# Optimization experiments

Hardware: AMD Instinct MI355X
Metric: run time of the kernel (lower is better)

Reference implementation:

```python
import jax, jax.numpy as jnp
import numpy as np

B, T, H = 2, 2048, 1024
NH_R, HD_R = 4, 256            # RWKV6 heads / head_dim
EXP, HD_M = 2, 64
DI = EXP * H                   # mamba inner = 2048
NH_M = DI // HD_M              # 32 mamba heads
DS = 128                       # mamba d_state
CK = 4                         # causal conv kernel
FFN = 4 * H
EPS = 1e-6


def rms(x, w, eps=EPS):
    return w * x * jax.lax.rsqrt(jnp.mean(x * x, -1, keepdims=True) + eps)


def setup_inputs() -> dict:
    key = jax.random.key(0)
    ks = iter(jax.random.split(key, 32))
    def w(shape, scale=0.02):
        return jax.random.normal(next(ks), shape, jnp.float32) * scale
    return dict(
        x=w((B, T, H), 1.0),
        ln_w=jnp.ones((H,), jnp.float32),
        r_w=w((H, H)), k_w=w((H, H)), v_w=w((H, H)), g_w=w((H, H)), dw_w=w((H, H)),
        u=w((NH_R, HD_R), 0.5),
        gn_w=jnp.ones((H,), jnp.float32),
        o_w=w((H, H)),
        in_proj=w((H, 2 * DI + 2 * DS + NH_M)),
        conv_w=w((DI + 2 * DS, CK), 0.1),
        conv_b=jnp.zeros((DI + 2 * DS,), jnp.float32),
        dt_bias=w((NH_M,), 0.1),
        A_log=jnp.log(jnp.arange(1, NH_M + 1, dtype=jnp.float32)),
        D_m=w((NH_M,), 0.5),
        m_norm_w=jnp.ones((DI,), jnp.float32),
        out_proj=w((DI, H)),
        gate_w=jnp.zeros((2 * H, 1), jnp.float32),   # zero-init per module
        gate_b=jnp.zeros((1,), jnp.float32),         # logit(0.5) = 0
        ffn_ln_w=jnp.ones((H,), jnp.float32),
        ffn_w1=w((H, FFN)),
        ffn_w2=w((FFN, H)),
    )


def _rwkv6(nx, r_w, k_w, v_w, g_w, dw_w, u, gn_w, o_w):
    r = (nx @ r_w).reshape(B, T, NH_R, HD_R)
    k = (nx @ k_w).reshape(B, T, NH_R, HD_R)
    v = (nx @ v_w).reshape(B, T, NH_R, HD_R)
    g = jax.nn.silu(nx @ g_w)                                  # output gate
    wdec = jnp.exp(-jnp.exp(nx @ dw_w)).reshape(B, T, NH_R, HD_R)  # data-dep decay in (0,1)
    tm = lambda a: a.transpose(1, 0, 2, 3)                     # [T,B,h,d]

    def step(S, inp):  # S: [B,h,K,V]
        rt, kt, vt, wt = inp
        kv = kt[..., :, None] * vt[..., None, :]
        o = jnp.einsum('bhk,bhkv->bhv', rt, S + u[..., :, None] * kv)
        return wt[..., :, None] * S + kv, o

    S0 = jnp.zeros((B, NH_R, HD_R, HD_R), nx.dtype)
    _, o = jax.lax.scan(step, S0, (tm(r), tm(k), tm(v), tm(wdec)))
    o = o.transpose(1, 0, 2, 3)                                # [B,T,h,d]
    o = o * jax.lax.rsqrt(jnp.mean(o * o, -1, keepdims=True) + EPS)  # per-head RMS (group norm)
    o = o.reshape(B, T, H) * gn_w
    return (o * g) @ o_w


def _mamba2(nx, in_proj, conv_w, conv_b, dt_bias, A_log, D_m, m_norm_w, out_proj):
    zxbcdt = nx @ in_proj
    z, xBC, dt = jnp.split(zxbcdt, [DI, 2 * DI + 2 * DS], axis=-1)
    xp = jnp.pad(xBC, ((0, 0), (CK - 1, 0), (0, 0)))           # causal depthwise conv
    xBC = sum(xp[:, i:i + T, :] * conv_w[:, i] for i in range(CK)) + conv_b
    xBC = jax.nn.silu(xBC)
    xm, Bm, Cm = jnp.split(xBC, [DI, DI + DS], axis=-1)
    xm = xm.reshape(B, T, NH_M, HD_M)
    dt = jax.nn.softplus(dt + dt_bias)                          # [B,T,nh]
    A = -jnp.exp(A_log)                                         # [nh]

    def step(h, inp):  # h: [B,nh,hd,ds]
        xt, Bt, Ct, dtt = inp
        h = h * jnp.exp(dtt * A)[..., None, None] + (dtt[..., None] * xt)[..., None] * Bt[:, None, None, :]
        y = jnp.einsum('bhds,bs->bhd', h, Ct)
        return h, y

    h0 = jnp.zeros((B, NH_M, HD_M, DS), nx.dtype)
    _, y = jax.lax.scan(step, h0, (xm.transpose(1, 0, 2, 3), Bm.transpose(1, 0, 2), Cm.transpose(1, 0, 2), dt.transpose(1, 0, 2)))
    y = y.transpose(1, 0, 2, 3) + D_m[None, None, :, None] * xm
    y = y.reshape(B, T, DI)
    y = rms(y * jax.nn.silu(z), m_norm_w)                       # gated RMSNorm
    return y @ out_proj


def reference(x, ln_w, r_w, k_w, v_w, g_w, dw_w, u, gn_w, o_w,
              in_proj, conv_w, conv_b, dt_bias, A_log, D_m, m_norm_w, out_proj,
              gate_w, gate_b, ffn_ln_w, ffn_w1, ffn_w2):
    nx = rms(x, ln_w)
    o_r = _rwkv6(nx, r_w, k_w, v_w, g_w, dw_w, u, gn_w, o_w)
    o_m = _mamba2(nx, in_proj, conv_w, conv_b, dt_bias, A_log, D_m, m_norm_w, out_proj)
    gate = jax.nn.sigmoid(jnp.concatenate([o_r, o_m], -1) @ gate_w + gate_b)  # [B,T,1]
    x = x + gate * o_r + (1.0 - gate) * o_m
    x = x + jax.nn.gelu(rms(x, ffn_ln_w) @ ffn_w1, approximate=False) @ ffn_w2
    return x
```

## Files before the change

kernel.cpp:

```cpp
#include <hip/hip_runtime.h>
#include <hip/hip_bf16.h>
#include <stdint.h>

#define B_ 2
#define T_ 2048
#define H_ 1024
#define M_ 4096
#define DI 2048
#define DS 128
#define CONVD 2304
#define LD2 4480
#define EPS_ 1e-6f

typedef __bf16 bf16x8 __attribute__((ext_vector_type(8)));
typedef float f32x4 __attribute__((ext_vector_type(4)));
typedef uint32_t u32x4 __attribute__((ext_vector_type(4)));

__device__ __forceinline__ unsigned short f2bfu(float f) {
    union { float f; uint32_t u; } a; a.f = f;
    uint32_t r = a.u + 0x7FFFu + ((a.u >> 16) & 1u);
    return (unsigned short)(r >> 16);
}
__device__ __forceinline__ float bfu2f(unsigned short u) {
    union { uint32_t u; float f; } a; a.u = ((uint32_t)u) << 16; return a.f;
}
__device__ __forceinline__ float siluf(float x) { return x / (1.f + expf(-x)); }
__device__ __forceinline__ bf16x8 zero8() { bf16x8 r{}; return r; }

__global__ __launch_bounds__(256) void k_rms1024(const float* __restrict__ in, const float* __restrict__ w,
                                                 unsigned short* __restrict__ out) {
    __shared__ float red[4];
    int m = blockIdx.x, tid = threadIdx.x;
    size_t base = (size_t)m * H_ + tid * 4;
    float4 v = *(const float4*)(in + base);
    float ss = v.x * v.x + v.y * v.y + v.z * v.z + v.w * v.w;
#pragma unroll
    for (int off = 32; off; off >>= 1) ss += __shfl_xor(ss, off);
    if ((tid & 63) == 0) red[tid >> 6] = ss;
    __syncthreads();
    float scale = rsqrtf((red[0] + red[1] + red[2] + red[3]) * (1.f / 1024.f) + EPS_);
    float4 wv = *(const float4*)(w + tid * 4);
    ushort4 o;
    o.x = f2bfu(v.x * wv.x * scale); o.y = f2bfu(v.y * wv.y * scale);
    o.z = f2bfu(v.z * wv.z * scale); o.w = f2bfu(v.w * wv.w * scale);
    *(ushort4*)(out + base) = o;
}

__global__ __launch_bounds__(256) void k_transpose(const float* __restrict__ src, unsigned short* __restrict__ dst,
                                                   int K, int N, int NP) {
    __shared__ float t[32][33];
    int n0 = blockIdx.x * 32, k0 = blockIdx.y * 32;
    int tx = threadIdx.x & 31, ty = threadIdx.x >> 5;
#pragma unroll
    for (int i = ty; i < 32; i += 8) {
        int k = k0 + i, n = n0 + tx;
        t[i][tx] = (n < N) ? src[(size_t)k * N + n] : 0.f;
    }
    __syncthreads();
#pragma unroll
    for (int i = ty; i < 32; i += 8) {
        int n = n0 + i, k = k0 + tx;
        if (n < NP) dst[(size_t)n * K + k] = f2bfu(t[tx][i]);
    }
}

template <int EPI>
__global__ __launch_bounds__(256) void k_gemm(const unsigned short* __restrict__ A, const unsigned short* __restrict__ Bt,
                                              void* __restrict__ Cout, const float* __restrict__ aux,
                                              int M, int N, int K) {
    __shared__ alignas(16) unsigned short As[128 * 64];
    __shared__ alignas(16) unsigned short Bs[128 * 64];
    const int tid = threadIdx.x;
    const int m0 = blockIdx.y * 128, n0 = blockIdx.x * 128;
    const int wave = tid >> 6, lane = tid & 63;
    const int wm = (wave >> 1) * 64, wn = (wave & 1) * 64;
    const int fr = lane & 15, fg = lane >> 4;
    const int srow = tid >> 3;
    const int ske = (tid & 7) * 8;

    f32x4 acc[4][4];
#pragma unroll
    for (int m = 0; m < 4; m++)
#pragma unroll
        for (int n = 0; n < 4; n++) acc[m][n] = (f32x4)(0.f);

    const int nk = K >> 6;
    u32x4 ra[4], rb[4];
#pragma unroll
    for (int i = 0; i < 4; i++) {
        ra[i] = *(const u32x4*)(A + (size_t)(m0 + srow + 32 * i) * K + ske);
        rb[i] = *(const u32x4*)(Bt + (size_t)(n0 + srow + 32 * i) * K + ske);
    }
    for (int kt = 0; kt < nk; ++kt) {
        __syncthreads();
#pragma unroll
        for (int i = 0; i < 4; i++) {
            int lin = (tid + 256 * i) * 16;
            int sw = lin ^ (((lin >> 7) & 7) << 4);
            *(u32x4*)((char*)As + sw) = ra[i];
            *(u32x4*)((char*)Bs + sw) = rb[i];
        }
        __syncthreads();
        if (kt + 1 < nk) {
#pragma unroll
            for (int i = 0; i < 4; i++) {
                ra[i] = *(const u32x4*)(A + (size_t)(m0 + srow + 32 * i) * K + (kt + 1) * 64 + ske);
                rb[i] = *(const u32x4*)(Bt + (size_t)(n0 + srow + 32 * i) * K + (kt + 1) * 64 + ske);
            }
        }
#pragma unroll
        for (int ks = 0; ks < 2; ++ks) {
            bf16x8 af[4], bg[4];
#pragma unroll
            for (int m = 0; m < 4; m++) {
                int row = wm + m * 16 + fr;
                int lin = row * 128 + ks * 64 + fg * 16;
                af[m] = *(const bf16x8*)((const char*)As + (lin ^ ((row & 7) << 4)));
            }
#pragma unroll
            for (int n = 0; n < 4; n++) {
                int col = wn + n * 16 + fr;
                int lin = col * 128 + ks * 64 + fg * 16;
                bg[n] = *(const bf16x8*)((const char*)Bs + (lin ^ ((col & 7) << 4)));
            }
#pragma unroll
            for (int m = 0; m < 4; m++)
#pragma unroll
                for (int n = 0; n < 4; n++)
                    acc[m][n] = __builtin_amdgcn_mfma_f32_16x16x32_bf16(af[m], bg[n], acc[m][n], 0, 0, 0);
        }
    }
#pragma unroll
    for (int m = 0; m < 4; m++) {
#pragma unroll
        for (int r = 0; r < 4; r++) {
            size_t row = (size_t)(m0 + wm + m * 16 + fg * 4 + r);
#pragma unroll
            for (int n = 0; n < 4; n++) {
                size_t idx = row * N + n0 + wn + n * 16 + fr;
                float v = acc[m][n][r];
                if constexpr (EPI == 0) ((float*)Cout)[idx] = v;
                else if constexpr (EPI == 4) ((unsigned short*)Cout)[idx] = f2bfu(0.5f * v * (1.f + erff(v * 0.70710678118f)));
                else ((float*)Cout)[idx] = v + aux[idx];
            }
        }
    }
}

__global__ __launch_bounds__(256) void k_gemm_fused(const unsigned short* __restrict__ A, const unsigned short* __restrict__ Bt,
                                                    unsigned short* __restrict__ RB, unsigned short* __restrict__ KB,
                                                    unsigned short* __restrict__ VB, unsigned short* __restrict__ GB,
                                                    float* __restrict__ WF, unsigned short* __restrict__ C2B) {
    __shared__ alignas(16) unsigned short As[128 * 64];
    __shared__ alignas(16) unsigned short Bs[128 * 64];
    const int tid = threadIdx.x;
    const int m0 = blockIdx.y * 128, n0 = blockIdx.x * 128;
    const int wave = tid >> 6, lane = tid & 63;
    const int wm = (wave >> 1) * 64, wn = (wave & 1) * 64;
    const int fr = lane & 15, fg = lane >> 4;
    const int srow = tid >> 3;
    const int ske = (tid & 7) * 8;
    const int K = 1024;

    f32x4 acc[4][4];
#pragma unroll
    for (int m = 0; m < 4; m++)
#pragma unroll
        for (int n = 0; n < 4; n++) acc[m][n] = (f32x4)(0.f);

    u32x4 ra[4], rb[4];
#pragma unroll
    for (int i = 0; i < 4; i++) {
        ra[i] = *(const u32x4*)(A + (size_t)(m0 + srow + 32 * i) * K + ske);
        rb[i] = *(const u32x4*)(Bt + (size_t)(n0 + srow + 32 * i) * K + ske);
    }
    for (int kt = 0; kt < 16; ++kt) {
        __syncthreads();
#pragma unroll
        for (int i = 0; i < 4; i++) {
            int lin = (tid + 256 * i) * 16;
            int sw = lin ^ (((lin >> 7) & 7) << 4);
            *(u32x4*)((char*)As + sw) = ra[i];
            *(u32x4*)((char*)Bs + sw) = rb[i];
        }
        __syncthreads();
        if (kt + 1 < 16) {
#pragma unroll
            for (int i = 0; i < 4; i++) {
                ra[i] = *(const u32x4*)(A + (size_t)(m0 + srow + 32 * i) * K + (kt + 1) * 64 + ske);
                rb[i] = *(const u32x4*)(Bt + (size_t)(n0 + srow + 32 * i) * K + (kt + 1) * 64 + ske);
            }
        }
#pragma unroll
        for (int ks = 0; ks < 2; ++ks) {
            bf16x8 af[4], bg[4];
#pragma unroll
            for (int m = 0; m < 4; m++) {
                int row = wm + m * 16 + fr;
                int lin = row * 128 + ks * 64 + fg * 16;
                af[m] = *(const bf16x8*)((const char*)As + (lin ^ ((row & 7) << 4)));
            }
#pragma unroll
            for (int n = 0; n < 4; n++) {
                int col = wn + n * 16 + fr;
                int lin = col * 128 + ks * 64 + fg * 16;
                bg[n] = *(const bf16x8*)((const char*)Bs + (lin ^ ((col & 7) << 4)));
            }
#pragma unroll
            for (int m = 0; m < 4; m++)
#pragma unroll
                for (int n = 0; n < 4; n++)
                    acc[m][n] = __builtin_amdgcn_mfma_f32_16x16x32_bf16(af[m], bg[n], acc[m][n], 0, 0, 0);
        }
    }
    const int seg = n0 >> 10;
#pragma unroll
    for (int m = 0; m < 4; m++) {
#pragma unroll
        for (int r = 0; r < 4; r++) {
            size_t row = (size_t)(m0 + wm + m * 16 + fg * 4 + r);
#pragma unroll
            for (int n = 0; n < 4; n++) {
                int gcol = n0 + wn + n * 16 + fr;
                float v = acc[m][n][r];
                if (n0 < 5120) {
                    size_t idx = row * 1024 + (gcol & 1023);
                    if (seg == 0) RB[idx] = f2bfu(v);
                    else if (seg == 1) KB[idx] = f2bfu(v);
                    else if (seg == 2) VB[idx] = f2bfu(v);
                    else if (seg == 3) GB[idx] = f2bfu(siluf(v));
                    else WF[idx] = expf(-expf(v));
                } else {
                    C2B[row * 4480 + (gcol - 5120)] = f2bfu(v);
                }
            }
        }
    }
}

__global__ __launch_bounds__(256) void k_rwkv_prep(unsigned short* __restrict__ RB, unsigned short* __restrict__ KB,
                                                   const float* __restrict__ WF, const float* __restrict__ u,
                                                   unsigned short* __restrict__ KDt, unsigned short* __restrict__ QLb,
                                                   float* __restrict__ DDb) {
    __shared__ float red[16][257];
    __shared__ float red2[16][17];
    const int c = blockIdx.x, bh = blockIdx.y;
    const int b = bh >> 2, h = bh & 3;
    const int k = threadIdx.x;
    const size_t m0 = (size_t)b * T_ + c * 16;
    const int hk = h * 256 + k;
    const float uv = u[hk];
    float Q = 1.f;
    float kd[16];
#pragma unroll
    for (int s = 0; s < 16; s++) {
        size_t off = (m0 + s) * H_ + hk;
        float r = bfu2f(RB[off]);
        float kv = bfu2f(KB[off]);
        float w = WF[off];
        RB[off] = f2bfu(r * Q);
        Q = fmaxf(Q * w, 1e-35f);
        float kdv = kv / Q;
        kd[s] = kdv;
        KB[off] = f2bfu(kdv);
        red[s][k] = r * uv * kv;
    }
    QLb[((size_t)(b * 128 + c)) * 1024 + hk] = f2bfu(Q);
    size_t kt0 = (((size_t)(b * 128 + c)) * 1024 + hk) * 16;
#pragma unroll
    for (int s = 0; s < 16; s++) KDt[kt0 + s] = f2bfu(kd[s]);
    __syncthreads();
    {
        int s = threadIdx.x >> 4, part = threadIdx.x & 15;
        float ps = 0.f;
#pragma unroll
        for (int j = 0; j < 16; j++) ps += red[s][part * 16 + j];
        red2[s][part] = ps;
    }
    __syncthreads();
    if (threadIdx.x < 32) {
        int s = threadIdx.x & 15, half = threadIdx.x >> 4;
        float d = 0.f;
#pragma unroll
        for (int j = 0; j < 8; j++) d += red2[s][half * 8 + j];
        DDb[(((size_t)bh * 128 + c) * 2 + half) * 16 + s] = d;
    }
}

__global__ __launch_bounds__(256) void k_rwkv_carry(const unsigned short* __restrict__ KD, const unsigned short* __restrict__ VB,
                                                    const unsigned short* __restrict__ QLb, unsigned short* __restrict__ Scc) {
    __shared__ unsigned short kds[16][256];
    __shared__ float lv[16][4];
    const int vg = blockIdx.x, bh = blockIdx.y;
    const int b = bh >> 2, h = bh & 3;
    const int k = threadIdx.x;
    const int hk = h * 256 + k;
    const size_t baseM = (size_t)b * T_;
    float s0 = 0.f, s1 = 0.f, s2 = 0.f, s3 = 0.f;
    for (int c = 0; c < 128; ++c) {
        size_t m0 = baseM + c * 16;
        if ((c & 7) == 0 && c > 0) {
            int cc = c >> 3;
            size_t sb = ((size_t)(bh * 16 + cc) * 256 + vg * 4) * 256 + k;
            Scc[sb] = f2bfu(s0); Scc[sb + 256] = f2bfu(s1);
            Scc[sb + 512] = f2bfu(s2); Scc[sb + 768] = f2bfu(s3);
        }
        __syncthreads();
#pragma unroll
        for (int it = 0; it < 2; ++it) {
            int i = threadIdx.x + it * 256;
            int row = i >> 5, col8 = (i & 31) * 8;
            *(u32x4*)&kds[row][col8] = *(const u32x4*)(KD + (m0 + row) * H_ + h * 256 + col8);
        }
        if (threadIdx.x < 64) {
            int t = threadIdx.x >> 2, j = threadIdx.x & 3;
            lv[t][j] = bfu2f(VB[(m0 + t) * H_ + h * 256 + vg * 4 + j]);
        }
        __syncthreads();
        float a0 = 0.f, a1 = 0.f, a2 = 0.f, a3 = 0.f;
#pragma unroll
        for (int t = 0; t < 16; t++) {
            float kdv = bfu2f(kds[t][k]);
            a0 = fmaf(kdv, lv[t][0], a0);
            a1 = fmaf(kdv, lv[t][1], a1);
            a2 = fmaf(kdv, lv[t][2], a2);
            a3 = fmaf(kdv, lv[t][3], a3);
        }
        float ql = bfu2f(QLb[((size_t)(b * 128 + c)) * 1024 + hk]);
        s0 = (s0 + a0) * ql; s1 = (s1 + a1) * ql;
        s2 = (s2 + a2) * ql; s3 = (s3 + a3) * ql;
    }
}

__global__ __launch_bounds__(256) void k_rwkv_out(const unsigned short* __restrict__ RT, const unsigned short* __restrict__ KD,
                                                  const unsigned short* __restrict__ KDt, const unsigned short* __restrict__ VB,
                                                  const unsigned short* __restrict__ QLb, const float* __restrict__ DDb,
                                                  const unsigned short* __restrict__ Scc,
                                                  float* __restrict__ P0, float* __restrict__ P1) {
    __shared__ unsigned short Sb[64][136];
    __shared__ unsigned short VT[64][24];
    __shared__ unsigned short Ab[16][24];
    __shared__ float dls[16];
    const int tid = threadIdx.x;
    const int vt = blockIdx.x, cc = blockIdx.y;
    const int bh = blockIdx.z >> 1, kh = blockIdx.z & 1;
    const int b = bh >> 2, h = bh & 3;
    const int wave = tid >> 6, lane = tid & 63;
    const int l16 = lane & 15, lq = lane >> 4;
    const int wv0 = wave * 16;
    const int hk0 = h * 256 + kh * 128;
    const int hv = h * 256 + vt * 64;
    const int aoff = (lq < 2) ? lq * 8 : 0;
    float* __restrict__ OP = kh ? P1 : P0;
    f32x4 sreg[8];
    if (cc == 0) {
#pragma unroll
        for (int kt = 0; kt < 8; kt++) sreg[kt] = (f32x4)(0.f);
        for (int i = tid; i < 64 * 136 / 8; i += 256) ((u32x4*)Sb)[i] = (u32x4)(0u);
    } else {
        size_t sbase = ((size_t)(bh * 16 + cc) * 256 + vt * 64);
        for (int i = tid; i < 1024; i += 256) {
            int v = i >> 4, k8 = (i & 15) * 8;
            *(u32x4*)&Sb[v][k8] = *(const u32x4*)(Scc + (sbase + v) * 256 + kh * 128 + k8);
        }
#pragma unroll
        for (int kt = 0; kt < 8; kt++) {
            ushort4 w4 = *(const ushort4*)(Scc + (sbase + wv0 + l16) * 256 + kh * 128 + kt * 16 + lq * 4);
            sreg[kt][0] = bfu2f(w4.x); sreg[kt][1] = bfu2f(w4.y);
            sreg[kt][2] = bfu2f(w4.z); sreg[kt][3] = bfu2f(w4.w);
        }
    }
    __syncthreads();

    for (int fc = 0; fc < 8; ++fc) {
        const int c = cc * 8 + fc;
        const size_t m0 = (size_t)b * T_ + c * 16;
        const size_t bc = (size_t)(b * 128 + c);
        if (fc > 0) __syncthreads();
        {
            int st = tid >> 4, v4 = (tid & 15) * 4;
            ushort4 v4v = *(const ushort4*)(VB + (m0 + st) * H_ + hv + v4);
            VT[v4 + 0][st] = v4v.x; VT[v4 + 1][st] = v4v.y;
            VT[v4 + 2][st] = v4v.z; VT[v4 + 3][st] = v4v.w;
            if (tid < 16) dls[tid] = DDb[(((size_t)bh * 128 + c) * 2 + kh) * 16 + tid];
        }
        __syncthreads();
        const size_t rowA = (m0 + l16) * H_ + hk0;
        bf16x8 rtf[4];
#pragma unroll
        for (int ks = 0; ks < 4; ks++) rtf[ks] = *(const bf16x8*)(RT + rowA + ks * 32 + lq * 8);
        f32x4 Aacc = (f32x4)(0.f);
#pragma unroll
        for (int ks = 0; ks < 4; ks++) {
            bf16x8 kdf = *(const bf16x8*)(KD + rowA + ks * 32 + lq * 8);
            Aacc = __builtin_amdgcn_mfma_f32_16x16x32_bf16(rtf[ks], kdf, Aacc, 0, 0, 0);
        }
        f32x4 oacc = (f32x4)(0.f);
#pragma unroll
        for (int ks = 0; ks < 4; ks++) {
            bf16x8 sbf = *(const bf16x8*)(&Sb[wv0 + l16][ks * 32 + lq * 8]);
            oacc = __builtin_amdgcn_mfma_f32_16x16x32_bf16(rtf[ks], sbf, oacc, 0, 0, 0);
        }
#pragma unroll
        for (int r = 0; r < 4; r++) {
            int t = lq * 4 + r, s = l16;
            float av = (s < t) ? Aacc[r] : ((s == t) ? dls[t] : 0.f);
            Ab[t][s] = f2bfu(av);
        }
        bf16x8 abf_t = *(const bf16x8*)(&Ab[l16][aoff]);
        bf16x8 vtf_t = *(const bf16x8*)(&VT[wv0 + l16][aoff]);
        bf16x8 abf = (lq < 2) ? abf_t : zero8();
        bf16x8 vtf = (lq < 2) ? vtf_t : zero8();
        oacc = __builtin_amdgcn_mfma_f32_16x16x32_bf16(abf, vtf, oacc, 0, 0, 0);
#pragma unroll
        for (int r = 0; r < 4; r++)
            OP[(m0 + lq * 4 + r) * H_ + hv + wv0 + l16] = oacc[r];
#pragma unroll
        for (int kt = 0; kt < 8; kt++) {
            const unsigned short* kp = KDt + (((bc * 1024) + hk0 + kt * 16 + l16) << 4) + aoff;
            bf16x8 kdtf_t = *(const bf16x8*)kp;
            bf16x8 kdtf = (lq < 2) ? kdtf_t : zero8();
            sreg[kt] = __builtin_amdgcn_mfma_f32_16x16x32_bf16(kdtf, vtf, sreg[kt], 0, 0, 0);
            ushort4 q4 = *(const ushort4*)(QLb + bc * 1024 + hk0 + kt * 16 + lq * 4);
            sreg[kt][0] *= bfu2f(q4.x); sreg[kt][1] *= bfu2f(q4.y);
            sreg[kt][2] *= bfu2f(q4.z); sreg[kt][3] *= bfu2f(q4.w);
            ushort4 pk;
            pk.x = f2bfu(sreg[kt][0]); pk.y = f2bfu(sreg[kt][1]);
            pk.z = f2bfu(sreg[kt][2]); pk.w = f2bfu(sreg[kt][3]);
            *(ushort4*)(&Sb[wv0 + l16][kt * 16 + lq * 4]) = pk;
        }
    }
}

__global__ __launch_bounds__(256) void k_rwkv_post(const float* __restrict__ P0, const float* __restrict__ P1,
                                                   const float* __restrict__ gn_w, unsigned short* __restrict__ g_io) {
    int m = blockIdx.x, tid = threadIdx.x;
    int wave = tid >> 6, lane = tid & 63;
    size_t base = (size_t)m * H_ + wave * 256 + lane * 4;
    int col = wave * 256 + lane * 4;
    float4 a = *(const float4*)(P0 + base);
    float4 b4 = *(const float4*)(P1 + base);
    float4 v; v.x = a.x + b4.x; v.y = a.y + b4.y; v.z = a.z + b4.z; v.w = a.w + b4.w;
    float ss = v.x * v.x + v.y * v.y + v.z * v.z + v.w * v.w;
#pragma unroll
    for (int off = 32; off; off >>= 1) ss += __shfl_xor(ss, off);
    float scale = rsqrtf(ss * (1.f / 256.f) + EPS_);
    float4 gn = *(const float4*)(gn_w + col);
    ushort4 gb4 = *(const ushort4*)(g_io + base);
    ushort4 out;
    out.x = f2bfu(v.x * scale * gn.x * bfu2f(gb4.x));
    out.y = f2bfu(v.y * scale * gn.y * bfu2f(gb4.y));
    out.z = f2bfu(v.z * scale * gn.z * bfu2f(gb4.z));
    out.w = f2bfu(v.w * scale * gn.w * bfu2f(gb4.w));
    *(ushort4*)(g_io + base) = out;
}

__global__ __launch_bounds__(256) void k_conv(const unsigned short* __restrict__ C2B, const float* __restrict__ conv_w,
                                              const float* __restrict__ conv_b, unsigned short* __restrict__ XB,
                                              float* __restrict__ BCF) {
    int m = blockIdx.y;
    int c = blockIdx.x * 256 + threadIdx.x;
    int b = m >> 11, t = m & 2047;
    float acc = conv_b[c];
#pragma unroll
    for (int i = 0; i < 4; i++) {
        int tt = t - 3 + i;
        if (tt >= 0) acc = fmaf(bfu2f(C2B[((size_t)(b * T_ + tt)) * LD2 + DI + c]), conv_w[c * 4 + i], acc);
    }
    float r = siluf(acc);
    if (c < DI) XB[(size_t)m * DI + c] = f2bfu(r);
    else BCF[(size_t)m * 256 + (c - DI)] = r;
}

#define MT 32
__global__ __launch_bounds__(256, 2) void k_mamba_scan(const unsigned short* __restrict__ C2B, const unsigned short* __restrict__ XB,
                                                       const float* __restrict__ BCF,
                                                       const float* __restrict__ dt_bias, const float* __restrict__ A_log,
                                                       unsigned short* __restrict__ Y0, unsigned short* __restrict__ Y1) {
    __shared__ float lB[MT][68], lC[MT][68], lx[MT][16], lda[MT], ldt[MT];
    __shared__ float pst[MT * 272];
    const int tid = threadIdx.x;
    const int d0 = blockIdx.x * 16;
    const int sh = blockIdx.y;
    const int bh = blockIdx.z;
    const int b = bh >> 5, h = bh & 31;
    const int wave = tid >> 6, lane = tid & 63;
    const int dloc = wave * 4 + (lane >> 4);
    const int li = lane & 15;
    const size_t baseM = (size_t)b * T_;
    const float A = -expf(A_log[h]);
    const float dtb = dt_bias[h];
    unsigned short* __restrict__ YP = sh ? Y1 : Y0;
    float hS[4] = {0.f, 0.f, 0.f, 0.f};

    for (int c = 0; c < T_ / MT; ++c) {
        __syncthreads();
        int t0 = c * MT;
#pragma unroll
        for (int it = 0; it < 2; ++it) {
            int idx = (tid + it * 256) * 4;
            int tt = idx >> 6, s = idx & 63;
            const float* src = BCF + (baseM + t0 + tt) * 256 + sh * 64 + s;
            *(float4*)&lB[tt][s] = *(const float4*)(src);
            *(float4*)&lC[tt][s] = *(const float4*)(src + 128);
        }
#pragma unroll
        for (int it = 0; it < 2; ++it) {
            int idx = tid + it * 256;
            int tt = idx >> 4, i = idx & 15;
            lx[tt][i] = bfu2f(XB[(baseM + t0 + tt) * DI + h * 64 + d0 + i]);
        }
        if (tid < MT) {
            float draw = bfu2f(C2B[(baseM + t0 + tid) * LD2 + 4352 + h]) + dtb;
            float ds = draw > 20.f ? draw : log1pf(expf(draw));
            ldt[tid] = ds;
            lda[tid] = expf(A * ds);
        }
        __syncthreads();
#pragma unroll 1
        for (int tt = 0; tt < MT; ++tt) {
            float da = lda[tt];
            float dtx = ldt[tt] * lx[tt][dloc];
            float4 Bv = *(const float4*)&lB[tt][li * 4];
            float4 Cv = *(const float4*)&lC[tt][li * 4];
            hS[0] = fmaf(hS[0], da, dtx * Bv.x);
            hS[1] = fmaf(hS[1], da, dtx * Bv.y);
            hS[2] = fmaf(hS[2], da, dtx * Bv.z);
            hS[3] = fmaf(hS[3], da, dtx * Bv.w);
            float p0 = fmaf(hS[1], Cv.y, hS[0] * Cv.x);
            float p1 = fmaf(hS[3], Cv.w, hS[2] * Cv.z);
            pst[tt * 272 + dloc * 17 + li] = p0 + p1;
        }
        __syncthreads();
        {
            int tt = tid >> 3, dl = tid & 7;
            const float* row0 = &pst[tt * 272 + dl * 17];
            const float* row1 = &pst[tt * 272 + (dl + 8) * 17];
            float s0 = 0.f, s1 = 0.f;
#pragma unroll
            for (int j = 0; j < 16; j++) { s0 += row0[j]; s1 += row1[j]; }
            size_t orow = (baseM + t0 + tt) * DI + h * 64 + d0;
            YP[orow + dl] = f2bfu(s0);
            YP[orow + dl + 8] = f2bfu(s1);
        }
    }
}

__global__ __launch_bounds__(256) void k_mamba_post(unsigned short* __restrict__ y_io, const unsigned short* __restrict__ y1,
                                                    const unsigned short* __restrict__ XB,
                                                    const unsigned short* __restrict__ C2B, const float* __restrict__ D_m,
                                                    const float* __restrict__ mnw) {
    __shared__ float red[4];
    int m = blockIdx.x, tid = threadIdx.x;
    int j0 = tid * 8;
    const float Dv = D_m[j0 >> 6];
    ushort4 ya = *(const ushort4*)(y_io + (size_t)m * DI + j0);
    ushort4 yb = *(const ushort4*)(y_io + (size_t)m * DI + j0 + 4);
    ushort4 wa = *(const ushort4*)(y1 + (size_t)m * DI + j0);
    ushort4 wb = *(const ushort4*)(y1 + (size_t)m * DI + j0 + 4);
    ushort4 xa = *(const ushort4*)(XB + (size_t)m * DI + j0);
    ushort4 xb = *(const ushort4*)(XB + (size_t)m * DI + j0 + 4);
    ushort4 za = *(const ushort4*)(C2B + (size_t)m * LD2 + j0);
    ushort4 zb = *(const ushort4*)(C2B + (size_t)m * LD2 + j0 + 4);
    float yv[8] = {bfu2f(ya.x) + bfu2f(wa.x), bfu2f(ya.y) + bfu2f(wa.y), bfu2f(ya.z) + bfu2f(wa.z), bfu2f(ya.w) + bfu2f(wa.w),
                   bfu2f(yb.x) + bfu2f(wb.x), bfu2f(yb.y) + bfu2f(wb.y), bfu2f(yb.z) + bfu2f(wb.z), bfu2f(yb.w) + bfu2f(wb.w)};
    float xv[8] = {bfu2f(xa.x), bfu2f(xa.y), bfu2f(xa.z), bfu2f(xa.w), bfu2f(xb.x), bfu2f(xb.y), bfu2f(xb.z), bfu2f(xb.w)};
    float zv[8] = {bfu2f(za.x), bfu2f(za.y), bfu2f(za.z), bfu2f(za.w), bfu2f(zb.x), bfu2f(zb.y), bfu2f(zb.z), bfu2f(zb.w)};
    float val[8];
    float ss = 0.f;
#pragma unroll
    for (int i = 0; i < 8; i++) {
        float v = (yv[i] + Dv * xv[i]) * siluf(zv[i]);
        val[i] = v;
        ss += v * v;
    }
#pragma unroll
    for (int off = 32; off; off >>= 1) ss += __shfl_xor(ss, off);
    if ((tid & 63) == 0) red[tid >> 6] = ss;
    __syncthreads();
    float scale = rsqrtf((red[0] + red[1] + red[2] + red[3]) * (1.f / 2048.f) + EPS_);
    ushort4 oa, ob;
    oa.x = f2bfu(val[0] * scale * mnw[j0 + 0]); oa.y = f2bfu(val[1] * scale * mnw[j0 + 1]);
    oa.z = f2bfu(val[2] * scale * mnw[j0 + 2]); oa.w = f2bfu(val[3] * scale * mnw[j0 + 3]);
    ob.x = f2bfu(val[4] * scale * mnw[j0 + 4]); ob.y = f2bfu(val[5] * scale * mnw[j0 + 5]);
    ob.z = f2bfu(val[6] * scale * mnw[j0 + 6]); ob.w = f2bfu(val[7] * scale * mnw[j0 + 7]);
    *(ushort4*)(y_io + (size_t)m * DI + j0) = oa;
    *(ushort4*)(y_io + (size_t)m * DI + j0 + 4) = ob;
}

__global__ __launch_bounds__(256) void k_mix(const float* __restrict__ x, const float* __restrict__ o_r,
                                             const float* __restrict__ o_m, const float* __restrict__ gw,
                                             const float* __restrict__ gb, const float* __restrict__ flnw,
                                             float* __restrict__ x1, unsigned short* __restrict__ nx2) {
    __shared__ float red[4];
    int m = blockIdx.x, tid = threadIdx.x;
    size_t base = (size_t)m * H_ + tid * 4;
    float4 orv = *(const float4*)(o_r + base);
    float4 omv = *(const float4*)(o_m + base);
    float4 xv = *(const float4*)(x + base);
    float4 g1 = *(const float4*)(gw + tid * 4);
    float4 g2 = *(const float4*)(gw + 1024 + tid * 4);
    float ps = orv.x * g1.x + orv.y * g1.y + orv.z * g1.z + orv.w * g1.w
             + omv.x * g2.x + omv.y * g2.y + omv.z * g2.z + omv.w * g2.w;
#pragma unroll
    for (int off = 32; off; off >>= 1) ps += __shfl_xor(ps, off);
    if ((tid & 63) == 0) red[tid >> 6] = ps;
    __syncthreads();
    float g = 1.f / (1.f + expf(-(red[0] + red[1] + red[2] + red[3] + gb[0])));
    float4 xo;
    xo.x = xv.x + g * orv.x + (1.f - g) * omv.x;
    xo.y = xv.y + g * orv.y + (1.f - g) * omv.y;
    xo.z = xv.z + g * orv.z + (1.f - g) * omv.z;
    xo.w = xv.w + g * orv.w + (1.f - g) * omv.w;
    *(float4*)(x1 + base) = xo;
    float ss = xo.x * xo.x + xo.y * xo.y + xo.z * xo.z + xo.w * xo.w;
#pragma unroll
    for (int off = 32; off; off >>= 1) ss += __shfl_xor(ss, off);
    __syncthreads();
    if ((tid & 63) == 0) red[tid >> 6] = ss;
    __syncthreads();
    float scale = rsqrtf((red[0] + red[1] + red[2] + red[3]) * (1.f / 1024.f) + EPS_);
    float4 wv = *(const float4*)(flnw + tid * 4);
    ushort4 o;
    o.x = f2bfu(xo.x * scale * wv.x); o.y = f2bfu(xo.y * scale * wv.y);
    o.z = f2bfu(xo.z * scale * wv.z); o.w = f2bfu(xo.w * scale * wv.w);
    *(ushort4*)(nx2 + base) = o;
}

extern "C" void kernel_launch(void* const* d_in, const int* in_sizes, int n_in,
                              void* d_out, int out_size, void* d_ws, size_t ws_size,
                              hipStream_t stream) {
    const float* x = (const float*)d_in[0];
    const float* ln_w = (const float*)d_in[1];
    const float* r_w = (const float*)d_in[2];
    const float* k_w = (const float*)d_in[3];
    const float* v_w = (const float*)d_in[4];
    const float* g_w = (const float*)d_in[5];
    const float* dw_w = (const float*)d_in[6];
    const float* u = (const float*)d_in[7];
    const float* gn_w = (const float*)d_in[8];
    const float* o_w = (const float*)d_in[9];
    const float* in_proj = (const float*)d_in[10];
    const float* conv_w = (const float*)d_in[11];
    const float* conv_b = (const float*)d_in[12];
    const float* dt_bias = (const float*)d_in[13];
    const float* A_log = (const float*)d_in[14];
    const float* D_m = (const float*)d_in[15];
    const float* m_norm_w = (const float*)d_in[16];
    const float* out_proj = (const float*)d_in[17];
    const float* gate_w = (const float*)d_in[18];
    const float* gate_b = (const float*)d_in[19];
    const float* ffn_ln_w = (const float*)d_in[20];
    const float* ffn_w1 = (const float*)d_in[21];
    const float* ffn_w2 = (const float*)d_in[22];
    (void)in_sizes; (void)n_in;

    const size_t NEEDED = 192675840ull;
    if (ws_size < NEEDED) {
        hipMemsetAsync(d_out, 0, (size_t)out_size * 4, stream);
        return;
    }
    char* ws = (char*)d_ws;
    unsigned short* WT5 = (unsigned short*)(ws + 0);
    unsigned short* INPT = (unsigned short*)(ws + 10485760);
    unsigned short* QLb = (unsigned short*)(ws + 0);
    float* DDb = (float*)(ws + 524288);
    unsigned short* SCC = (unsigned short*)(ws + 1048576);
    unsigned short* F1T = (unsigned short*)(ws + 0);
    unsigned short* F2T = (unsigned short*)(ws + 10485760);
    unsigned short* OWT = (unsigned short*)(ws + 19660800);
    unsigned short* OPT = (unsigned short*)(ws + 21757952);
    unsigned short* NXB = (unsigned short*)(ws + 25952256);
    unsigned short* KDt = NXB;
    unsigned short* RB = (unsigned short*)(ws + 34340864);
    unsigned short* KB = (unsigned short*)(ws + 42729472);
    unsigned short* VB = (unsigned short*)(ws + 51118080);
    unsigned short* GB = (unsigned short*)(ws + 59506688);
    float* WF = (float*)(ws + 67895296);
    unsigned short* Y1 = (unsigned short*)(ws + 67895296);
    float* OM = (float*)(ws + 34340864);
    unsigned short* MIDB = (unsigned short*)(ws + 51118080);
    unsigned short* C2B = (unsigned short*)(ws + 84672512);
    unsigned short* XB = (unsigned short*)(ws + 121372672);
    float* BCF = (float*)(ws + 138149888);
    float* P0 = (float*)(ws + 142344192);
    float* P1 = (float*)(ws + 159121408);
    unsigned short* YB = (unsigned short*)(ws + 175898624);

    dim3 blk(256);
    k_rms1024<<<M_, blk, 0, stream>>>(x, ln_w, NXB);
    k_transpose<<<dim3(32, 32), blk, 0, stream>>>(r_w, WT5 + 0ull * 1048576, 1024, 1024, 1024);
    k_transpose<<<dim3(32, 32), blk, 0, stream>>>(k_w, WT5 + 1ull * 1048576, 1024, 1024, 1024);
    k_transpose<<<dim3(32, 32), blk, 0, stream>>>(v_w, WT5 + 2ull * 1048576, 1024, 1024, 1024);
    k_transpose<<<dim3(32, 32), blk, 0, stream>>>(g_w, WT5 + 3ull * 1048576, 1024, 1024, 1024);
    k_transpose<<<dim3(32, 32), blk, 0, stream>>>(dw_w, WT5 + 4ull * 1048576, 1024, 1024, 1024);
    k_transpose<<<dim3(140, 32), blk, 0, stream>>>(in_proj, INPT, 1024, 4384, 4480);
    k_transpose<<<dim3(32, 32), blk, 0, stream>>>(o_w, OWT, 1024, 1024, 1024);
    k_transpose<<<dim3(32, 64), blk, 0, stream>>>(out_proj, OPT, 2048, 1024, 1024);
    k_gemm_fused<<<dim3(75, 32), blk, 0, stream>>>(NXB, WT5, RB, KB, VB, GB, WF, C2B);
    k_conv<<<dim3(9, M_), blk, 0, stream>>>(C2B, conv_w, conv_b, XB, BCF);
    k_rwkv_prep<<<dim3(128, 8), blk, 0, stream>>>(RB, KB, WF, u, KDt, QLb, DDb);
    k_rwkv_carry<<<dim3(64, 8), blk, 0, stream>>>(KB, VB, QLb, SCC);
    k_rwkv_out<<<dim3(4, 16, 16), blk, 0, stream>>>(RB, KB, KDt, VB, QLb, DDb, SCC, P0, P1);
    k_rwkv_post<<<M_, blk, 0, stream>>>(P0, P1, gn_w, GB);
    k_transpose<<<dim3(128, 32), blk, 0, stream>>>(ffn_w1, F1T, 1024, 4096, 4096);
    k_transpose<<<dim3(32, 128), blk, 0, stream>>>(ffn_w2, F2T, 4096, 1024, 1024);
    k_mamba_scan<<<dim3(4, 2, 64), blk, 0, stream>>>(C2B, XB, BCF, dt_bias, A_log, YB, Y1);
    k_mamba_post<<<M_, blk, 0, stream>>>(YB, Y1, XB, C2B, D_m, m_norm_w);
    k_gemm<0><<<dim3(8, 32), blk, 0, stream>>>(GB, OWT, P1, nullptr, 4096, 1024, 1024);
    k_gemm<0><<<dim3(8, 32), blk, 0, stream>>>(YB, OPT, OM, nullptr, 4096, 1024, 2048);
    k_mix<<<M_, blk, 0, stream>>>(x, P1, OM, gate_w, gate_b, ffn_ln_w, P0, NXB);
    k_gemm<4><<<dim3(32, 32), blk, 0, stream>>>(NXB, F1T, MIDB, nullptr, 4096, 4096, 1024);
    k_gemm<5><<<dim3(8, 32), blk, 0, stream>>>(MIDB, F2T, (float*)d_out, P0, 4096, 1024, 4096);
}
```

Measured before the change: 1.053 ms.

## Replace sequential Mamba2 scan with chunked SSD matmul formulation on MFMA

Replaces the per-timestep recurrent Mamba2 scan with a chunked state-space-duality scheme. A prep kernel computes cumulative dt and decay factors, a mask kernel builds the intra-chunk C·B^T decay matrices with MFMA, a carry kernel computes chunk-boundary states, and an output kernel combines the inter-chunk state contribution with the intra-chunk attention-like term using bf16 MFMA. The aim is to swap the long serial FMA loop for parallel matrix-core work. In exchange it adds more launches, intermediate buffers, and bf16 rounding of states and decay-weighted terms.

```diff
diff --git a/kernel.cpp b/kernel.cpp
--- a/kernel.cpp
+++ b/kernel.cpp
@@ -472,81 +472,279 @@
     else BCF[(size_t)m * 256 + (c - DI)] = r;
 }
 
-#define MT 32
-__global__ __launch_bounds__(256, 2) void k_mamba_scan(const unsigned short* __restrict__ C2B, const unsigned short* __restrict__ XB,
-                                                       const float* __restrict__ BCF,
-                                                       const float* __restrict__ dt_bias, const float* __restrict__ A_log,
-                                                       unsigned short* __restrict__ Y0, unsigned short* __restrict__ Y1) {
-    __shared__ float lB[MT][68], lC[MT][68], lx[MT][16], lda[MT], ldt[MT];
-    __shared__ float pst[MT * 272];
+__global__ __launch_bounds__(256) void k_mprep(const unsigned short* __restrict__ C2B,
+                                               const float* __restrict__ dt_bias, const float* __restrict__ A_log,
+                                               float* __restrict__ DT, float* __restrict__ CD,
+                                               float* __restrict__ WS, float* __restrict__ WSC,
+                                               float* __restrict__ QJ, float* __restrict__ QLf,
+                                               float* __restrict__ QC) {
+    __shared__ float sums[128], offs[128], ce[16];
+    const int bh = blockIdx.x;
+    const int b = bh >> 5, h = bh & 31;
+    const int c = threadIdx.x;
+    const float A = -expf(A_log[h]);
+    const float dtb = dt_bias[h];
+    float dloc[16], cdl[16];
+    if (c < 128) {
+        float acc = 0.f;
+#pragma unroll
+        for (int s = 0; s < 16; s++) {
+            size_t m = (size_t)b * T_ + c * 16 + s;
+            float draw = bfu2f(C2B[m * LD2 + 4352 + h]) + dtb;
+            float dt = draw > 20.f ? draw : log1pf(expf(draw));
+            acc += dt;
+            dloc[s] = dt; cdl[s] = acc;
+        }
+        sums[c] = acc;
+    }
+    __syncthreads();
+    if (threadIdx.x == 0) {
+        float run = 0.f;
+        for (int i = 0; i < 128; i++) { offs[i] = run; run += sums[i]; }
+    }
+    __syncthreads();
+    if (threadIdx.x < 16) {
+        int last = threadIdx.x * 8 + 7;
+        ce[threadIdx.x] = offs[last] + sums[last];
+    }
+    __syncthreads();
+    if (c < 128) {
+        float off = offs[c];
+        float cd15 = off + cdl[15];
+        float ceC = ce[c >> 3];
+        QLf[bh * 128 + c] = expf(fminf(A * cdl[15], 0.f));
+        size_t base = (size_t)bh * 2048 + c * 16;
+#pragma unroll
+        for (int s = 0; s < 16; s++) {
+            float cdg = off + cdl[s];
+            DT[base + s] = dloc[s];
+            CD[base + s] = cdg;
+            QJ[base + s] = expf(fminf(A * (cdg - off), 0.f));
+            WS[base + s] = expf(fminf(A * (cd15 - cdg), 0.f)) * dloc[s];
+            WSC[base + s] = expf(fminf(A * (ceC - cdg), 0.f)) * dloc[s];
+        }
+    }
+    if (threadIdx.x < 16) {
+        float prev = threadIdx.x ? ce[threadIdx.x - 1] : 0.f;
+        QC[bh * 16 + threadIdx.x] = expf(fminf(A * (ce[threadIdx.x] - prev), 0.f));
+    }
+}
+
+__global__ __launch_bounds__(64) void k_amask(const float* __restrict__ BCF,
+                                              const float* __restrict__ CD, const float* __restrict__ DT,
+                                              const float* __restrict__ A_log,
+                                              unsigned short* __restrict__ AM) {
+    const int c = blockIdx.x, bh = blockIdx.y;
+    const int b = bh >> 5, h = bh & 31;
+    const int lane = threadIdx.x;
+    const int l16 = lane & 15, lq = lane >> 4;
+    const float A = -expf(A_log[h]);
+    const size_t m = (size_t)b * T_ + c * 16 + l16;
+    f32x4 Aacc = (f32x4)(0.f);
+#pragma unroll
+    for (int ks = 0; ks < 4; ks++) {
+        bf16x8 cf, bf;
+        const float* cr = BCF + m * 256 + 128 + ks * 32 + lq * 8;
+        const float* br = BCF + m * 256 + ks * 32 + lq * 8;
+#pragma unroll
+        for (int i = 0; i < 8; i++) { cf[i] = (__bf16)cr[i]; bf[i] = (__bf16)br[i]; }
+        Aacc = __builtin_amdgcn_mfma_f32_16x16x32_bf16(cf, bf, Aacc, 0, 0, 0);
+    }
+    size_t base = ((size_t)bh * 128 + c) * 256;
+    size_t tb = (size_t)bh * 2048 + c * 16;
+    float cds = CD[tb + l16];
+    float dts = DT[tb + l16];
+#pragma unroll
+    for (int r = 0; r < 4; r++) {
+        int j = lq * 4 + r;
+        float av = 0.f;
+        if (l16 <= j) {
+            float cdj = CD[tb + j];
+            av = Aacc[r] * expf(fminf(A * (cdj - cds), 0.f)) * dts;
+        }
+        AM[base + j * 16 + l16] = f2bfu(av);
+    }
+}
+
+__global__ __launch_bounds__(256) void k_mcarry(const float* __restrict__ BCF, const unsigned short* __restrict__ XB,
+                                                const float* __restrict__ WSC, const float* __restrict__ QC,
+                                                unsigned short* __restrict__ MSCC) {
+    __shared__ float Bsf[64][128];
+    __shared__ unsigned short BWt[128][72];
+    __shared__ unsigned short XT[16][72];
+    __shared__ float wsl[64];
     const int tid = threadIdx.x;
-    const int d0 = blockIdx.x * 16;
-    const int sh = blockIdx.y;
-    const int bh = blockIdx.z;
+    const int dq = blockIdx.x, bh = blockIdx.y;
     const int b = bh >> 5, h = bh & 31;
     const int wave = tid >> 6, lane = tid & 63;
-    const int dloc = wave * 4 + (lane >> 4);
-    const int li = lane & 15;
+    const int l16 = lane & 15, lq = lane >> 4;
     const size_t baseM = (size_t)b * T_;
-    const float A = -expf(A_log[h]);
-    const float dtb = dt_bias[h];
-    unsigned short* __restrict__ YP = sh ? Y1 : Y0;
-    float hS[4] = {0.f, 0.f, 0.f, 0.f};
-
-    for (int c = 0; c < T_ / MT; ++c) {
+    f32x4 sreg[2];
+    sreg[0] = (f32x4)(0.f); sreg[1] = (f32x4)(0.f);
+
+    for (int cc = 0; cc < 15; ++cc) {
+        float qC = QC[bh * 16 + cc];
+        sreg[0] *= qC; sreg[1] *= qC;
+        for (int sub = 0; sub < 2; ++sub) {
+            int t0g = cc * 128 + sub * 64;
+            __syncthreads();
+            if (tid < 64) wsl[tid] = WSC[(size_t)bh * 2048 + t0g + tid];
+#pragma unroll
+            for (int i = 0; i < 8; i++) {
+                int idx4 = tid + i * 256;
+                int t = idx4 >> 5, s4 = (idx4 & 31) * 4;
+                *(float4*)&Bsf[t][s4] = *(const float4*)(BCF + (baseM + t0g + t) * 256 + s4);
+            }
+#pragma unroll
+            for (int i = 0; i < 4; i++) {
+                int idx = tid + i * 256;
+                int t = idx >> 4, d = idx & 15;
+                XT[d][t] = XB[(baseM + t0g + t) * DI + h * 64 + dq * 16 + d];
+            }
+            __syncthreads();
+            {
+                int sg = tid >> 1;
+                int tb = (tid & 1) * 32;
+#pragma unroll
+                for (int q = 0; q < 8; q++) {
+                    int tt = tb + q * 4;
+                    ushort4 v;
+                    v.x = f2bfu(Bsf[tt + 0][sg] * wsl[tt + 0]);
+                    v.y = f2bfu(Bsf[tt + 1][sg] * wsl[tt + 1]);
+                    v.z = f2bfu(Bsf[tt + 2][sg] * wsl[tt + 2]);
+                    v.w = f2bfu(Bsf[tt + 3][sg] * wsl[tt + 3]);
+                    *(ushort4*)&BWt[sg][tt] = v;
+                }
+            }
+            __syncthreads();
+#pragma unroll
+            for (int st = 0; st < 2; st++) {
+#pragma unroll
+                for (int ks = 0; ks < 2; ks++) {
+                    bf16x8 bwf = *(const bf16x8*)&BWt[wave * 32 + st * 16 + l16][ks * 32 + lq * 8];
+                    bf16x8 xtf = *(const bf16x8*)&XT[l16][ks * 32 + lq * 8];
+                    sreg[st] = __builtin_amdgcn_mfma_f32_16x16x32_bf16(bwf, xtf, sreg[st], 0, 0, 0);
+                }
+            }
+        }
+        size_t dbase = ((size_t)(bh * 16 + cc + 1) * 64 + dq * 16 + l16) * 128;
+#pragma unroll
+        for (int st = 0; st < 2; st++) {
+            ushort4 pk;
+            pk.x = f2bfu(sreg[st][0]); pk.y = f2bfu(sreg[st][1]);
+            pk.z = f2bfu(sreg[st][2]); pk.w = f2bfu(sreg[st][3]);
+            *(ushort4*)(MSCC + dbase + wave * 32 + st * 16 + lq * 4) = pk;
+        }
+    }
+}
+
+__global__ __launch_bounds__(256) void k_mout(const float* __restrict__ BCF, const unsigned short* __restrict__ XB,
+                                              const unsigned short* __restrict__ AM,
+                                              const float* __restrict__ QJ, const float* __restrict__ WS,
+                                              const float* __restrict__ QLf, const unsigned short* __restrict__ MSCC,
+                                              unsigned short* __restrict__ Y) {
+    __shared__ unsigned short Sb[64][136];
+    __shared__ unsigned short Cs[16][136];
+    __shared__ unsigned short BWt[128][24];
+    __shared__ unsigned short XT[64][24];
+    __shared__ unsigned short Ab[16][24];
+    __shared__ float qjl[16], wsl[16], qLl;
+    const int tid = threadIdx.x;
+    const int cc = blockIdx.x, bh = blockIdx.y;
+    const int b = bh >> 5, h = bh & 31;
+    const int wave = tid >> 6, lane = tid & 63;
+    const int l16 = lane & 15, lq = lane >> 4;
+    const int wv0 = wave * 16;
+    const int aoff = (lq < 2) ? lq * 8 : 0;
+    const size_t baseM = (size_t)b * T_;
+    f32x4 sreg[8];
+    if (cc == 0) {
+#pragma unroll
+        for (int kt = 0; kt < 8; kt++) sreg[kt] = (f32x4)(0.f);
+        for (int i = tid; i < 64 * 136 / 8; i += 256) ((u32x4*)Sb)[i] = (u32x4)(0u);
+    } else {
+        size_t sbase = (size_t)(bh * 16 + cc) * 64;
+        for (int i = tid; i < 1024; i += 256) {
+            int d = i >> 4, s8 = (i & 15) * 8;
+            *(u32x4*)&Sb[d][s8] = *(const u32x4*)(MSCC + (sbase + d) * 128 + s8);
+        }
+#pragma unroll
+        for (int kt = 0; kt < 8; kt++) {
+            ushort4 w4 = *(const ushort4*)(MSCC + (sbase + wv0 + l16) * 128 + kt * 16 + lq * 4);
+            sreg[kt][0] = bfu2f(w4.x); sreg[kt][1] = bfu2f(w4.y);
+            sreg[kt][2] = bfu2f(w4.z); sreg[kt][3] = bfu2f(w4.w);
+        }
+    }
+
+    for (int fc = 0; fc < 8; ++fc) {
+        const int c = cc * 8 + fc;
+        const size_t m0 = baseM + c * 16;
         __syncthreads();
-        int t0 = c * MT;
-#pragma unroll
-        for (int it = 0; it < 2; ++it) {
-            int idx = (tid + it * 256) * 4;
-            int tt = idx >> 6, s = idx & 63;
-            const float* src = BCF + (baseM + t0 + tt) * 256 + sh * 64 + s;
-            *(float4*)&lB[tt][s] = *(const float4*)(src);
-            *(float4*)&lC[tt][s] = *(const float4*)(src + 128);
-        }
-#pragma unroll
-        for (int it = 0; it < 2; ++it) {
-            int idx = tid + it * 256;
-            int tt = idx >> 4, i = idx & 15;
-            lx[tt][i] = bfu2f(XB[(baseM + t0 + tt) * DI + h * 64 + d0 + i]);
-        }
-        if (tid < MT) {
-            float draw = bfu2f(C2B[(baseM + t0 + tid) * LD2 + 4352 + h]) + dtb;
-            float ds = draw > 20.f ? draw : log1pf(expf(draw));
-            ldt[tid] = ds;
-            lda[tid] = expf(A * ds);
+        if (tid < 16) {
+            size_t tb = (size_t)bh * 2048 + c * 16 + tid;
+            qjl[tid] = QJ[tb];
+            wsl[tid] = WS[tb];
+            if (tid == 0) qLl = QLf[bh * 128 + c];
+        }
+        {
+            int j = tid >> 4, s = tid & 15;
+            Ab[j][s] = AM[((size_t)bh * 128 + c) * 256 + tid];
+        }
+#pragma unroll
+        for (int i = 0; i < 8; i++) {
+            int idx = tid + i * 256;
+            int t = idx >> 7, sig = idx & 127;
+            Cs[t][sig] = f2bfu(BCF[(m0 + t) * 256 + 128 + sig]);
+        }
+#pragma unroll
+        for (int i = 0; i < 4; i++) {
+            int idx = tid + i * 256;
+            int t = idx >> 6, d = idx & 63;
+            XT[d][t] = XB[(m0 + t) * DI + h * 64 + d];
         }
         __syncthreads();
-#pragma unroll 1
-        for (int tt = 0; tt < MT; ++tt) {
-            float da = lda[tt];
-            float dtx = ldt[tt] * lx[tt][dloc];
-            float4 Bv = *(const float4*)&lB[tt][li * 4];
-            float4 Cv = *(const float4*)&lC[tt][li * 4];
-            hS[0] = fmaf(hS[0], da, dtx * Bv.x);
-            hS[1] = fmaf(hS[1], da, dtx * Bv.y);
-            hS[2] = fmaf(hS[2], da, dtx * Bv.z);
-            hS[3] = fmaf(hS[3], da, dtx * Bv.w);
-            float p0 = fmaf(hS[1], Cv.y, hS[0] * Cv.x);
-            float p1 = fmaf(hS[3], Cv.w, hS[2] * Cv.z);
-            pst[tt * 272 + dloc * 17 + li] = p0 + p1;
+#pragma unroll
+        for (int i = 0; i < 8; i++) {
+            int idx = tid + i * 256;
+            int t = idx >> 7, sig = idx & 127;
+            BWt[sig][t] = f2bfu(BCF[(m0 + t) * 256 + sig] * wsl[t]);
         }
         __syncthreads();
-        {
-            int tt = tid >> 3, dl = tid & 7;
-            const float* row0 = &pst[tt * 272 + dl * 17];
-            const float* row1 = &pst[tt * 272 + (dl + 8) * 17];
-            float s0 = 0.f, s1 = 0.f;
-#pragma unroll
-            for (int j = 0; j < 16; j++) { s0 += row0[j]; s1 += row1[j]; }
-            size_t orow = (baseM + t0 + tt) * DI + h * 64 + d0;
-            YP[orow + dl] = f2bfu(s0);
-            YP[orow + dl + 8] = f2bfu(s1);
-        }
-    }
-}
-
-__global__ __launch_bounds__(256) void k_mamba_post(unsigned short* __restrict__ y_io, const unsigned short* __restrict__ y1,
+        bf16x8 cf[4];
+#pragma unroll
+        for (int ks = 0; ks < 4; ks++) cf[ks] = *(const bf16x8*)(&Cs[l16][ks * 32 + lq * 8]);
+        f32x4 oacc = (f32x4)(0.f);
+#pragma unroll
+        for (int ks = 0; ks < 4; ks++) {
+            bf16x8 sbf = *(const bf16x8*)(&Sb[wv0 + l16][ks * 32 + lq * 8]);
+            oacc = __builtin_amdgcn_mfma_f32_16x16x32_bf16(cf[ks], sbf, oacc, 0, 0, 0);
+        }
+#pragma unroll
+        for (int r = 0; r < 4; r++) oacc[r] *= qjl[lq * 4 + r];
+        bf16x8 abf_t = *(const bf16x8*)(&Ab[l16][aoff]);
+        bf16x8 xtf_t = *(const bf16x8*)(&XT[wv0 + l16][aoff]);
+        bf16x8 abf = (lq < 2) ? abf_t : zero8();
+        bf16x8 xtf = (lq < 2) ? xtf_t : zero8();
+        oacc = __builtin_amdgcn_mfma_f32_16x16x32_bf16(abf, xtf, oacc, 0, 0, 0);
+#pragma unroll
+        for (int r = 0; r < 4; r++)
+            Y[(m0 + lq * 4 + r) * DI + h * 64 + wv0 + l16] = f2bfu(oacc[r]);
+        float qL = qLl;
+#pragma unroll
+        for (int kt = 0; kt < 8; kt++) {
+            sreg[kt] *= qL;
+            bf16x8 bwf_t = *(const bf16x8*)(&BWt[kt * 16 + l16][aoff]);
+            bf16x8 bwf = (lq < 2) ? bwf_t : zero8();
+            sreg[kt] = __builtin_amdgcn_mfma_f32_16x16x32_bf16(bwf, xtf, sreg[kt], 0, 0, 0);
+            ushort4 pk;
+            pk.x = f2bfu(sreg[kt][0]); pk.y = f2bfu(sreg[kt][1]);
+            pk.z = f2bfu(sreg[kt][2]); pk.w = f2bfu(sreg[kt][3]);
+            *(ushort4*)(&Sb[wv0 + l16][kt * 16 + lq * 4]) = pk;
+        }
+    }
+}
+
+__global__ __launch_bounds__(256) void k_mamba_post(unsigned short* __restrict__ y_io,
                                                     const unsigned short* __restrict__ XB,
                                                     const unsigned short* __restrict__ C2B, const float* __restrict__ D_m,
                                                     const float* __restrict__ mnw) {
@@ -556,14 +754,12 @@
     const float Dv = D_m[j0 >> 6];
     ushort4 ya = *(const ushort4*)(y_io + (size_t)m * DI + j0);
     ushort4 yb = *(const ushort4*)(y_io + (size_t)m * DI + j0 + 4);
-    ushort4 wa = *(const ushort4*)(y1 + (size_t)m * DI + j0);
-    ushort4 wb = *(const ushort4*)(y1 + (size_t)m * DI + j0 + 4);
     ushort4 xa = *(const ushort4*)(XB + (size_t)m * DI + j0);
     ushort4 xb = *(const ushort4*)(XB + (size_t)m * DI + j0 + 4);
     ushort4 za = *(const ushort4*)(C2B + (size_t)m * LD2 + j0);
     ushort4 zb = *(const ushort4*)(C2B + (size_t)m * LD2 + j0 + 4);
-    float yv[8] = {bfu2f(ya.x) + bfu2f(wa.x), bfu2f(ya.y) + bfu2f(wa.y), bfu2f(ya.z) + bfu2f(wa.z), bfu2f(ya.w) + bfu2f(wa.w),
-                   bfu2f(yb.x) + bfu2f(wb.x), bfu2f(yb.y) + bfu2f(wb.y), bfu2f(yb.z) + bfu2f(wb.z), bfu2f(yb.w) + bfu2f(wb.w)};
+    float yv[8] = {bfu2f(ya.x), bfu2f(ya.y), bfu2f(ya.z), bfu2f(ya.w),
+                   bfu2f(yb.x), bfu2f(yb.y), bfu2f(yb.z), bfu2f(yb.w)};
     float xv[8] = {bfu2f(xa.x), bfu2f(xa.y), bfu2f(xa.z), bfu2f(xa.w), bfu2f(xb.x), bfu2f(xb.y), bfu2f(xb.z), bfu2f(xb.w)};
     float zv[8] = {bfu2f(za.x), bfu2f(za.y), bfu2f(za.z), bfu2f(za.w), bfu2f(zb.x), bfu2f(zb.y), bfu2f(zb.z), bfu2f(zb.w)};
     float val[8];
@@ -666,6 +862,7 @@
     unsigned short* QLb = (unsigned short*)(ws + 0);
     float* DDb = (float*)(ws + 524288);
     unsigned short* SCC = (unsigned short*)(ws + 1048576);
+    unsigned short* MSCC = (unsigned short*)(ws + 1048576);
     unsigned short* F1T = (unsigned short*)(ws + 0);
     unsigned short* F2T = (unsigned short*)(ws + 10485760);
     unsigned short* OWT = (unsigned short*)(ws + 19660800);
@@ -677,7 +874,15 @@
     unsigned short* VB = (unsigned short*)(ws + 51118080);
     unsigned short* GB = (unsigned short*)(ws + 59506688);
     float* WF = (float*)(ws + 67895296);
-    unsigned short* Y1 = (unsigned short*)(ws + 67895296);
+    char* MTB = ws + 67895296;
+    float* DTt = (float*)(MTB + 0);
+    float* CDt = (float*)(MTB + 524288);
+    float* WSt = (float*)(MTB + 1048576);
+    float* WSCt = (float*)(MTB + 1572864);
+    float* QJt = (float*)(MTB + 2097152);
+    float* QLft = (float*)(MTB + 2621440);
+    float* QCt = (float*)(MTB + 2654208);
+    unsigned short* AMt = (unsigned short*)(MTB + 2658304);
     float* OM = (float*)(ws + 34340864);
     unsigned short* MIDB = (unsigned short*)(ws + 51118080);
     unsigned short* C2B = (unsigned short*)(ws + 84672512);
@@ -700,13 +905,16 @@
     k_gemm_fused<<<dim3(75, 32), blk, 0, stream>>>(NXB, WT5, RB, KB, VB, GB, WF, C2B);
     k_conv<<<dim3(9, M_), blk, 0, stream>>>(C2B, conv_w, conv_b, XB, BCF);
     k_rwkv_prep<<<dim3(128, 8), blk, 0, stream>>>(RB, KB, WF, u, KDt, QLb, DDb);
+    k_mprep<<<64, blk, 0, stream>>>(C2B, dt_bias, A_log, DTt, CDt, WSt, WSCt, QJt, QLft, QCt);
+    k_amask<<<dim3(128, 64), dim3(64), 0, stream>>>(BCF, CDt, DTt, A_log, AMt);
     k_rwkv_carry<<<dim3(64, 8), blk, 0, stream>>>(KB, VB, QLb, SCC);
     k_rwkv_out<<<dim3(4, 16, 16), blk, 0, stream>>>(RB, KB, KDt, VB, QLb, DDb, SCC, P0, P1);
     k_rwkv_post<<<M_, blk, 0, stream>>>(P0, P1, gn_w, GB);
+    k_mcarry<<<dim3(4, 64), blk, 0, stream>>>(BCF, XB, WSCt, QCt, MSCC);
+    k_mout<<<dim3(16, 64), blk, 0, stream>>>(BCF, XB, AMt, QJt, WSt, QLft, MSCC, YB);
+    k_mamba_post<<<M_, blk, 0, stream>>>(YB, XB, C2B, D_m, m_norm_w);
     k_transpose<<<dim3(128, 32), blk, 0, stream>>>(ffn_w1, F1T, 1024, 4096, 4096);
     k_transpose<<<dim3(32, 128), blk, 0, stream>>>(ffn_w2, F2T, 4096, 1024, 1024);
-    k_mamba_scan<<<dim3(4, 2, 64), blk, 0, stream>>>(C2B, XB, BCF, dt_bias, A_log, YB, Y1);
-    k_mamba_post<<<M_, blk, 0, stream>>>(YB, Y1, XB, C2B, D_m, m_norm_w);
     k_gemm<0><<<dim3(8, 32), blk, 0, stream>>>(GB, OWT, P1, nullptr, 4096, 1024, 1024);
     k_gemm<0><<<dim3(8, 32), blk, 0, stream>>>(YB, OPT, OM, nullptr, 4096, 1024, 2048);
     k_mix<<<M_, blk, 0, stream>>>(x, P1, OM, gate_w, gate_b, ffn_ln_w, P0, NXB);
```

Result: faster. 934.5 us, median of 2 (-11.3%).
